# Kernel tuning notes

Hardware: AMD Instinct MI355X
Metric: run time of the kernel (lower is better)

## Reference

```python
import jax, jax.numpy as jnp
import numpy as np

KV_POOL = 2


def setup_inputs() -> dict:
    key = jax.random.key(0)
    ks = jax.random.split(key, 12)
    B, C1, C2, H, W, D = 8, 256, 512, 64, 64, 64
    s = 0.02
    return {
        "x1": jax.random.normal(ks[0], (B, C1, H, W), jnp.float32),
        "x2": jax.random.normal(ks[1], (B, C2, H, W), jnp.float32),
        "Wq": jax.random.normal(ks[2], (D, C1), jnp.float32) * s,
        "bq": jnp.zeros((D,), jnp.float32),
        "Wk": jax.random.normal(ks[3], (D, C2), jnp.float32) * s,
        "bk": jnp.zeros((D,), jnp.float32),
        "Wv": jax.random.normal(ks[4], (D, C2), jnp.float32) * s,
        "bv": jnp.zeros((D,), jnp.float32),
        "Wo": jax.random.normal(ks[5], (C1, D), jnp.float32) * s,
        "bo": jnp.zeros((C1,), jnp.float32),
    }


def reference(x1, x2, Wq, bq, Wk, bk, Wv, bv, Wo, bo):
    B, C1, H, W = x1.shape
    D = Wq.shape[0]
    # adaptive_avg_pool2d to (H//2, W//2) with even dims == 2x2 mean pool
    Bs, C2, H2, W2 = x2.shape
    x2p = x2.reshape(Bs, C2, H2 // KV_POOL, KV_POOL, W2 // KV_POOL, KV_POOL).mean(axis=(3, 5))
    # 1x1 convs as channel matmuls; flatten spatial dims
    Q = jnp.einsum('bchw,dc->bhwd', x1, Wq).reshape(B, H * W, D) + bq          # [B,N,D]
    K = jnp.einsum('bchw,dc->bhwd', x2p, Wk).reshape(B, -1, D) + bk            # [B,M,D]
    V = jnp.einsum('bchw,dc->bhwd', x2p, Wv).reshape(B, -1, D) + bv            # [B,M,D]
    attn = jax.nn.softmax(jnp.einsum('bnd,bmd->bnm', Q, K), axis=-1)           # [B,N,M]
    out = jnp.einsum('bnm,bmd->bnd', attn, V)                                  # [B,N,D]
    y = jnp.einsum('bnd,cd->bnc', out, Wo) + bo                                # [B,N,C1]
    y = y.reshape(B, H, W, C1).transpose(0, 3, 1, 2)                           # [B,C1,H,W]
    return x1 + y
```

## Files before the change

kernel.cpp:

```cpp
#include <hip/hip_runtime.h>
#include <hip/hip_bf16.h>

typedef __bf16 bf16x4 __attribute__((ext_vector_type(4)));
typedef __bf16 bf16x8 __attribute__((ext_vector_type(8)));
typedef float f32x16 __attribute__((ext_vector_type(16)));
typedef unsigned int u32x4 __attribute__((ext_vector_type(4)));

static constexpr int Bc = 8, C1 = 256, C2 = 512, Hh = 64, Ww = 64, Dd = 64;
static constexpr int Nn = 4096, Mm = 1024;

#define MFMA __builtin_amdgcn_mfma_f32_32x32x16_bf16

__device__ __forceinline__ uint32_t pkbf(float a, float b) {
  union { __bf16 h[2]; uint32_t u; } x;
  x.h[0] = (__bf16)a; x.h[1] = (__bf16)b;
  return x.u;
}

__device__ __forceinline__ bf16x8 cvt8(const float* __restrict__ p) {
  float4 a = *(const float4*)p;
  float4 b2 = *(const float4*)(p + 4);
  bf16x8 r;
  r[0] = (__bf16)a.x; r[1] = (__bf16)a.y; r[2] = (__bf16)a.z; r[3] = (__bf16)a.w;
  r[4] = (__bf16)b2.x; r[5] = (__bf16)b2.y; r[6] = (__bf16)b2.z; r[7] = (__bf16)b2.w;
  return r;
}

__device__ __forceinline__ void pack16(const float* p, bf16x8& f0, bf16x8& f1) {
  uint32_t w01 = pkbf(p[0], p[1]),   w23 = pkbf(p[2], p[3]);
  uint32_t w45 = pkbf(p[4], p[5]),   w67 = pkbf(p[6], p[7]);
  uint32_t w89 = pkbf(p[8], p[9]),   wab = pkbf(p[10], p[11]);
  uint32_t wcd = pkbf(p[12], p[13]), wef = pkbf(p[14], p[15]);
  auto s0 = __builtin_amdgcn_permlane32_swap(w01, w45, false, false);
  auto s1 = __builtin_amdgcn_permlane32_swap(w23, w67, false, false);
  auto s2 = __builtin_amdgcn_permlane32_swap(w89, wcd, false, false);
  auto s3 = __builtin_amdgcn_permlane32_swap(wab, wef, false, false);
  u32x4 q0 = {s0[0], s1[0], s0[1], s1[1]};
  u32x4 q1 = {s2[0], s3[0], s2[1], s3[1]};
  f0 = __builtin_bit_cast(bf16x8, q0);
  f1 = __builtin_bit_cast(bf16x8, q1);
}

__global__ __launch_bounds__(256) void k_prep_w(
    const float* __restrict__ Wq, const float* __restrict__ Wk,
    const float* __restrict__ Wv, const float* __restrict__ Wo,
    __bf16* __restrict__ wqf, __bf16* __restrict__ wkf,
    __bf16* __restrict__ wvf, __bf16* __restrict__ wof) {
  int t = blockIdx.x * 256 + threadIdx.x;
  if (t < 2048) {
    int l = t & 63, g = t >> 6;
    int dh = g >> 4, ks = g & 15;
    int d = dh * 32 + (l & 31), c = ks * 16 + (l >> 5) * 8;
    *(bf16x8*)(wqf + (size_t)t * 8) = cvt8(Wq + (size_t)d * C1 + c);
  } else if (t < 6144) {
    int tt = t - 2048;
    int l = tt & 63, g = tt >> 6;
    int dh = g >> 5, ks = g & 31;
    int d = dh * 32 + (l & 31), c = ks * 16 + (l >> 5) * 8;
    *(bf16x8*)(wkf + (size_t)tt * 8) = cvt8(Wk + (size_t)d * C2 + c);
  } else if (t < 10240) {
    int tt = t - 6144;
    int l = tt & 63, g = tt >> 6;
    int dh = g >> 5, ks = g & 31;
    int d = dh * 32 + (l & 31), c = ks * 16 + (l >> 5) * 8;
    *(bf16x8*)(wvf + (size_t)tt * 8) = cvt8(Wv + (size_t)d * C2 + c);
  } else if (t < 12288) {
    int tt = t - 10240;
    int l = tt & 63, g = tt >> 6;
    int ct = g >> 2, ks = g & 3;
    int crow = ct * 32 + (l & 31), d = ks * 16 + (l >> 5) * 8;
    *(bf16x8*)(wof + (size_t)tt * 8) = cvt8(Wo + (size_t)crow * Dd + d);
  }
}

__global__ __launch_bounds__(256) void k_proj(
    const float* __restrict__ x1, const float* __restrict__ x2,
    const __bf16* __restrict__ wqf, const float* __restrict__ bq,
    const __bf16* __restrict__ wkf, const float* __restrict__ bk,
    const __bf16* __restrict__ wvf, const float* __restrict__ bv,
    __bf16* __restrict__ qfb, __bf16* __restrict__ kfb,
    __bf16* __restrict__ vfb) {
  __shared__ __align__(16) __bf16 lds[19392];
  const int bx = blockIdx.x, b = blockIdx.y, tid = threadIdx.x;
  const int w = tid >> 6, l = tid & 63, h = l >> 5, nl = l & 31;

  if (bx < 64) {
    const int n0 = bx * 64;
#pragma unroll 4
    for (int it = 0; it < 16; ++it) {
      int c = it * 16 + (tid >> 4);
      int q = tid & 15;
      float4 v = *(const float4*)(x1 + (size_t)(b * C1 + c) * Nn + n0 + 4 * q);
      lds[(4 * q + 0) * 266 + c] = (__bf16)v.x;
      lds[(4 * q + 1) * 266 + c] = (__bf16)v.y;
      lds[(4 * q + 2) * 266 + c] = (__bf16)v.z;
      lds[(4 * q + 3) * 266 + c] = (__bf16)v.w;
    }
    __syncthreads();
    const int nsub = w & 1, dh = w >> 1;
    const __bf16* arow = lds + (nsub * 32 + nl) * 266;
    const __bf16* wq8 = wqf + (size_t)dh * 16 * 512 + l * 8;
    f32x16 acc = {};
#pragma unroll
    for (int ks = 0; ks < 16; ++ks) {
      bf16x8 a = *(const bf16x8*)(arow + ks * 16 + 8 * h);
      bf16x8 bb = *(const bf16x8*)(wq8 + ks * 512);
      acc = MFMA(a, bb, acc, 0, 0, 0);
    }
    const int d = dh * 32 + nl;
    const float bias = bq[d];
    __bf16* qdst = qfb + (size_t)b * Nn * Dd + (size_t)((n0 >> 5) + nsub) * 2048 +
                   (d >> 4) * 512 + ((d >> 3) & 1) * 256 + (d & 7);
#pragma unroll
    for (int r = 0; r < 16; ++r) {
      int mrow = (r & 3) + 8 * (r >> 2) + 4 * h;
      qdst[mrow * 8] = (__bf16)(acc[r] + bias);
    }
  } else {
    const int h2 = bx - 64;
    __bf16* klds = lds;
    __bf16* vlds = lds + 32 * 522;
#pragma unroll 4
    for (int it = 0; it < 64; ++it) {
      int c = it * 8 + (tid >> 5);
      int j = tid & 31;
      const float* p = x2 + ((size_t)(b * C2 + c) * Hh + 2 * h2) * Ww + 2 * j;
      float2 v0 = *(const float2*)p;
      float2 v1 = *(const float2*)(p + Ww);
      klds[j * 522 + c] = (__bf16)((v0.x + v0.y + v1.x + v1.y) * 0.25f);
    }
    __syncthreads();
    const int isv = w >> 1, dh = w & 1;
    const __bf16* arow = klds + nl * 522;
    const __bf16* wf8 = (isv ? wvf : wkf) + (size_t)dh * 32 * 512 + l * 8;
    f32x16 acc = {};
#pragma unroll
    for (int ks = 0; ks < 32; ++ks) {
      bf16x8 a = *(const bf16x8*)(arow + ks * 16 + 8 * h);
      bf16x8 bb = *(const bf16x8*)(wf8 + ks * 512);
      acc = MFMA(a, bb, acc, 0, 0, 0);
    }
    const int d = dh * 32 + nl;
    const float bias = isv ? bv[d] : bk[d];
    if (!isv) {
      __bf16* kdst = kfb + (size_t)b * Mm * Dd + (size_t)h2 * 2048 +
                     (d >> 4) * 512 + ((d >> 3) & 1) * 256 + (d & 7);
#pragma unroll
      for (int r = 0; r < 16; ++r) {
        int mr = (r & 3) + 8 * (r >> 2) + 4 * h;
        kdst[mr * 8] = (__bf16)(acc[r] + bias);
      }
    } else {
#pragma unroll
      for (int r = 0; r < 16; ++r) {
        int mr = (r & 3) + 8 * (r >> 2) + 4 * h;
        vlds[d * 42 + mr] = (__bf16)(acc[r] + bias);
      }
    }
    __syncthreads();
    const int dd = tid >> 2, q = tid & 3;
    bf16x8 vv = *(const bf16x8*)(vlds + dd * 42 + q * 8);
    const int c = (q >> 1) * 2 + (dd >> 5);
    const int ll = (q & 1) * 32 + (dd & 31);
    *(bf16x8*)(vfb + (size_t)b * Mm * Dd + (size_t)h2 * 2048 + c * 512 + ll * 8) = vv;
  }
}

template <int S>
__global__ __launch_bounds__(256) void k_attn_part(
    const __bf16* __restrict__ qfb, const __bf16* __restrict__ kfb,
    const __bf16* __restrict__ vfb, __bf16* __restrict__ po,
    float* __restrict__ pml) {
  const int lin = blockIdx.x;
  const int b = lin & 7, rest = lin >> 3, nblk = rest & 31, sp = rest >> 5;
  const int tid = threadIdx.x;
  const int w = tid >> 6, l = tid & 63, h = l >> 5, nl = l & 31;
  const int n = nblk * 128 + w * 32 + nl;
  constexpr int NT = Mm / S / 32;
  const int t0 = sp * NT;

  const __bf16* qt = qfb + (size_t)b * Nn * Dd + (size_t)(nblk * 4 + w) * 2048 + l * 8;
  bf16x8 qf0 = *(const bf16x8*)(qt);
  bf16x8 qf1 = *(const bf16x8*)(qt + 512);
  bf16x8 qf2 = *(const bf16x8*)(qt + 1024);
  bf16x8 qf3 = *(const bf16x8*)(qt + 1536);

  const __bf16* kt = kfb + (size_t)b * Mm * Dd + (size_t)t0 * 2048 + l * 8;
  const __bf16* vt = vfb + (size_t)b * Mm * Dd + (size_t)t0 * 2048 + l * 8;

  f32x16 o0 = {}, o1 = {};
  float lsum = 0.f;

  bf16x8 ck0 = *(const bf16x8*)(kt);
  bf16x8 ck1 = *(const bf16x8*)(kt + 512);
  bf16x8 ck2 = *(const bf16x8*)(kt + 1024);
  bf16x8 ck3 = *(const bf16x8*)(kt + 1536);
  bf16x8 cv0 = *(const bf16x8*)(vt);
  bf16x8 cv1 = *(const bf16x8*)(vt + 512);
  bf16x8 cv2 = *(const bf16x8*)(vt + 1024);
  bf16x8 cv3 = *(const bf16x8*)(vt + 1536);

#pragma unroll
  for (int i = 0; i < NT; ++i) {
    bf16x8 nk0, nk1, nk2, nk3, nv0, nv1, nv2, nv3;
    if (i + 1 < NT) {
      const __bf16* kn = kt + (size_t)(i + 1) * 2048;
      const __bf16* vn = vt + (size_t)(i + 1) * 2048;
      nk0 = *(const bf16x8*)(kn);
      nk1 = *(const bf16x8*)(kn + 512);
      nk2 = *(const bf16x8*)(kn + 1024);
      nk3 = *(const bf16x8*)(kn + 1536);
      nv0 = *(const bf16x8*)(vn);
      nv1 = *(const bf16x8*)(vn + 512);
      nv2 = *(const bf16x8*)(vn + 1024);
      nv3 = *(const bf16x8*)(vn + 1536);
    }
    f32x16 s = {};
    s = MFMA(ck0, qf0, s, 0, 0, 0);
    s = MFMA(ck1, qf1, s, 0, 0, 0);
    s = MFMA(ck2, qf2, s, 0, 0, 0);
    s = MFMA(ck3, qf3, s, 0, 0, 0);
    float p[16];
#pragma unroll
    for (int r = 0; r < 16; ++r) p[r] = __expf(s[r]);
    float u0 = (p[0] + p[1]) + (p[2] + p[3]);
    float u1 = (p[4] + p[5]) + (p[6] + p[7]);
    float u2 = (p[8] + p[9]) + (p[10] + p[11]);
    float u3 = (p[12] + p[13]) + (p[14] + p[15]);
    lsum += (u0 + u1) + (u2 + u3);
    bf16x8 pb0, pb1;
    pack16(p, pb0, pb1);
    o0 = MFMA(cv0, pb0, o0, 0, 0, 0);
    o1 = MFMA(cv1, pb0, o1, 0, 0, 0);
    o0 = MFMA(cv2, pb1, o0, 0, 0, 0);
    o1 = MFMA(cv3, pb1, o1, 0, 0, 0);
    if (i + 1 < NT) {
      ck0 = nk0; ck1 = nk1; ck2 = nk2; ck3 = nk3;
      cv0 = nv0; cv1 = nv1; cv2 = nv2; cv3 = nv3;
    }
  }

  const float ltot = lsum + __shfl_xor(lsum, 32);
  __bf16* ob = po + (size_t)(b * S + sp) * 16 * Nn * 4 + (size_t)n * 4;
#pragma unroll
  for (int q = 0; q < 4; ++q) {
    bf16x4 t0v, t1v;
#pragma unroll
    for (int e = 0; e < 4; ++e) {
      t0v[e] = (__bf16)o0[q * 4 + e];
      t1v[e] = (__bf16)o1[q * 4 + e];
    }
    *(bf16x4*)(ob + (size_t)(2 * q + h) * Nn * 4) = t0v;
    *(bf16x4*)(ob + (size_t)(8 + 2 * q + h) * Nn * 4) = t1v;
  }
  if (h == 0) pml[(size_t)(b * S + sp) * Nn + n] = ltot;
}

template <int S>
__global__ __launch_bounds__(256) void k_attn_comb(
    const float* __restrict__ x1, const __bf16* __restrict__ po,
    const float* __restrict__ pml, const __bf16* __restrict__ wof,
    const float* __restrict__ bo, float* __restrict__ out) {
  const int lin = blockIdx.x;
  const int b = lin & 7, rest = lin >> 3, nblk = rest & 31, ctg = rest >> 5;
  const int tid = threadIdx.x;
  const int w = tid >> 6, l = tid & 63, h = l >> 5, nl = l & 31;
  const int n = nblk * 128 + w * 32 + nl;

  float L = 0.f;
#pragma unroll
  for (int s = 0; s < S; ++s)
    L += pml[(size_t)(b * S + s) * Nn + n];
  const float inv = 1.f / L;

  float o[32];
#pragma unroll
  for (int r = 0; r < 32; ++r) o[r] = 0.f;
#pragma unroll
  for (int s = 0; s < S; ++s) {
    const __bf16* ob = po + (size_t)(b * S + s) * 16 * Nn * 4 + (size_t)n * 4;
#pragma unroll
    for (int q = 0; q < 4; ++q) {
      bf16x4 v0 = *(const bf16x4*)(ob + (size_t)(2 * q + h) * Nn * 4);
      bf16x4 v1 = *(const bf16x4*)(ob + (size_t)(8 + 2 * q + h) * Nn * 4);
#pragma unroll
      for (int e = 0; e < 4; ++e) {
        o[q * 4 + e] += (float)v0[e];
        o[16 + q * 4 + e] += (float)v1[e];
      }
    }
  }

  bf16x8 obf[4];
#pragma unroll
  for (int a2 = 0; a2 < 2; ++a2) {
    float ov[16];
#pragma unroll
    for (int r = 0; r < 16; ++r) ov[r] = o[a2 * 16 + r] * inv;
    pack16(ov, obf[a2 * 2], obf[a2 * 2 + 1]);
  }

  const float* x1r = x1 + (size_t)b * C1 * Nn + n;
  float* outr = out + (size_t)b * C1 * Nn + n;
#pragma unroll
  for (int ci = 0; ci < 4; ++ci) {
    const int ct = ctg * 4 + ci;
    f32x16 y = {};
#pragma unroll
    for (int ks = 0; ks < 4; ++ks) {
      bf16x8 a = *(const bf16x8*)(wof + (size_t)((ct * 4 + ks) * 64 + l) * 8);
      y = MFMA(a, obf[ks], y, 0, 0, 0);
    }
#pragma unroll
    for (int r = 0; r < 16; ++r) {
      int c = ct * 32 + (r & 3) + 8 * (r >> 2) + 4 * h;
      size_t idx = (size_t)c * Nn;
      outr[idx] = y[r] + bo[c] + x1r[idx];
    }
  }
}

__global__ __launch_bounds__(256) void k_attn(
    const float* __restrict__ x1, const __bf16* __restrict__ qfb,
    const __bf16* __restrict__ kfb, const __bf16* __restrict__ vfb,
    const __bf16* __restrict__ wof, const float* __restrict__ bo,
    float* __restrict__ out) {
  const int b = blockIdx.y, tid = threadIdx.x;
  const int w = tid >> 6, l = tid & 63, h = l >> 5, nl = l & 31;
  const int n = blockIdx.x * 128 + w * 32 + nl;

  const __bf16* qt = qfb + (size_t)b * Nn * Dd + (size_t)(blockIdx.x * 4 + w) * 2048 + l * 8;
  bf16x8 qf0 = *(const bf16x8*)(qt);
  bf16x8 qf1 = *(const bf16x8*)(qt + 512);
  bf16x8 qf2 = *(const bf16x8*)(qt + 1024);
  bf16x8 qf3 = *(const bf16x8*)(qt + 1536);

  f32x16 o0 = {}, o1 = {};
  float mrun = -INFINITY, lsum = 0.f;

  const __bf16* kb_ = kfb + (size_t)b * Mm * Dd + l * 8;
  const __bf16* vb_ = vfb + (size_t)b * Mm * Dd + l * 8;

  for (int t = 0; t < 32; ++t) {
    const __bf16* kt = kb_ + (size_t)t * 2048;
    const __bf16* vt = vb_ + (size_t)t * 2048;
    bf16x8 ka0 = *(const bf16x8*)(kt);
    bf16x8 ka1 = *(const bf16x8*)(kt + 512);
    bf16x8 ka2 = *(const bf16x8*)(kt + 1024);
    bf16x8 ka3 = *(const bf16x8*)(kt + 1536);
    bf16x8 v00 = *(const bf16x8*)(vt);
    bf16x8 v10 = *(const bf16x8*)(vt + 512);
    bf16x8 v01 = *(const bf16x8*)(vt + 1024);
    bf16x8 v11 = *(const bf16x8*)(vt + 1536);
    f32x16 s = {};
    s = MFMA(ka0, qf0, s, 0, 0, 0);
    s = MFMA(ka1, qf1, s, 0, 0, 0);
    s = MFMA(ka2, qf2, s, 0, 0, 0);
    s = MFMA(ka3, qf3, s, 0, 0, 0);
    float tmax = s[0];
#pragma unroll
    for (int r = 1; r < 16; ++r) tmax = fmaxf(tmax, s[r]);
    tmax = fmaxf(tmax, __shfl_xor(tmax, 32));
    const float mnew = fmaxf(mrun, tmax);
    const float scale = __expf(mrun - mnew);
    float p[16], psum = 0.f;
#pragma unroll
    for (int r = 0; r < 16; ++r) { p[r] = __expf(s[r] - mnew); psum += p[r]; }
    lsum = lsum * scale + psum;
    mrun = mnew;
#pragma unroll
    for (int r = 0; r < 16; ++r) { o0[r] *= scale; o1[r] *= scale; }
    bf16x8 pb0, pb1;
    pack16(p, pb0, pb1);
    o0 = MFMA(v00, pb0, o0, 0, 0, 0);
    o1 = MFMA(v10, pb0, o1, 0, 0, 0);
    o0 = MFMA(v01, pb1, o0, 0, 0, 0);
    o1 = MFMA(v11, pb1, o1, 0, 0, 0);
  }

  const float ltot = lsum + __shfl_xor(lsum, 32);
  const float inv = 1.f / ltot;

  bf16x8 ob[4];
#pragma unroll
  for (int a2 = 0; a2 < 2; ++a2) {
    float ov[16];
#pragma unroll
    for (int r = 0; r < 16; ++r) ov[r] = (a2 ? o1[r] : o0[r]) * inv;
    pack16(ov, ob[a2 * 2], ob[a2 * 2 + 1]);
  }

  const float* x1r = x1 + (size_t)b * C1 * Nn + n;
  float* outr = out + (size_t)b * C1 * Nn + n;
#pragma unroll 2
  for (int ct = 0; ct < 8; ++ct) {
    f32x16 y = {};
#pragma unroll
    for (int ks = 0; ks < 4; ++ks) {
      bf16x8 a = *(const bf16x8*)(wof + (size_t)((ct * 4 + ks) * 64 + l) * 8);
      y = MFMA(a, ob[ks], y, 0, 0, 0);
    }
#pragma unroll
    for (int r = 0; r < 16; ++r) {
      int c = ct * 32 + (r & 3) + 8 * (r >> 2) + 4 * h;
      size_t idx = (size_t)c * Nn;
      outr[idx] = y[r] + bo[c] + x1r[idx];
    }
  }
}

extern "C" void kernel_launch(void* const* d_in, const int* in_sizes, int n_in,
                              void* d_out, int out_size, void* d_ws,
                              size_t ws_size, hipStream_t stream) {
  const float* x1 = (const float*)d_in[0];
  const float* x2 = (const float*)d_in[1];
  const float* Wq = (const float*)d_in[2];
  const float* bq = (const float*)d_in[3];
  const float* Wk = (const float*)d_in[4];
  const float* bk = (const float*)d_in[5];
  const float* Wv = (const float*)d_in[6];
  const float* bv = (const float*)d_in[7];
  const float* Wo = (const float*)d_in[8];
  const float* bo = (const float*)d_in[9];
  float* out = (float*)d_out;
  char* ws = (char*)d_ws;

  __bf16* wqf = (__bf16*)(ws);
  __bf16* wkf = (__bf16*)(ws + 32768);
  __bf16* wvf = (__bf16*)(ws + 98304);
  __bf16* wof = (__bf16*)(ws + 163840);
  __bf16* qfb = (__bf16*)(ws + 196608);
  __bf16* kfb = (__bf16*)(ws + 4390912);
  __bf16* vfb = (__bf16*)(ws + 5439488);
  __bf16* po  = (__bf16*)(ws + 6488064);
  const size_t ws8 = 6488064ull + 33554432ull + 1048576ull;
  const size_t ws4 = 6488064ull + 16777216ull + 524288ull;

  hipLaunchKernelGGL(k_prep_w, dim3(48), dim3(256), 0, stream,
                     Wq, Wk, Wv, Wo, wqf, wkf, wvf, wof);
  hipLaunchKernelGGL(k_proj, dim3(96, 8), dim3(256), 0, stream,
                     x1, x2, wqf, bq, wkf, bk, wvf, bv, qfb, kfb, vfb);
  if (ws_size >= ws8) {
    float* pml = (float*)(ws + 6488064 + 33554432);
    hipLaunchKernelGGL(k_attn_part<8>, dim3(32 * 8 * 8), dim3(256), 0, stream,
                       qfb, kfb, vfb, po, pml);
    hipLaunchKernelGGL(k_attn_comb<8>, dim3(32 * 8 * 2), dim3(256), 0, stream,
                       x1, po, pml, wof, bo, out);
  } else if (ws_size >= ws4) {
    float* pml = (float*)(ws + 6488064 + 16777216);
    hipLaunchKernelGGL(k_attn_part<4>, dim3(32 * 8 * 4), dim3(256), 0, stream,
                       qfb, kfb, vfb, po, pml);
    hipLaunchKernelGGL(k_attn_comb<4>, dim3(32 * 8 * 2), dim3(256), 0, stream,
                       x1, po, pml, wof, bo, out);
  } else {
    hipLaunchKernelGGL(k_attn, dim3(32, 8), dim3(256), 0, stream,
                       x1, qfb, kfb, vfb, wof, bo, out);
  }
}
```

Measured before the change: 63.36 us.

## Stage x1 and pooled x2 as bf16 MFMA fragments in a separate wide kernel

Adds a staging kernel that converts x1 and the 2x2-pooled x2 into bf16 fragment-ordered buffers across many small blocks, with weight prep folded into the same launch. The projection kernel then reads MFMA operands straight from global memory with no LDS transpose or syncthreads. The V output is packed with permlane swaps instead of going through LDS. The aim is more parallelism and less LDS traffic in the projection stage. The cost is an extra round trip of about 25MB of bf16 data through global memory and a larger workspace requirement, which may push execution onto the smaller-split fallback paths.

```diff
diff --git a/kernel.cpp b/kernel.cpp
--- a/kernel.cpp
+++ b/kernel.cpp
@@ -41,75 +41,124 @@
   f1 = __builtin_bit_cast(bf16x8, q1);
 }
 
-__global__ __launch_bounds__(256) void k_prep_w(
+
+__global__ __launch_bounds__(256) void k_stage(
+    const float* __restrict__ x1, const float* __restrict__ x2,
     const float* __restrict__ Wq, const float* __restrict__ Wk,
     const float* __restrict__ Wv, const float* __restrict__ Wo,
     __bf16* __restrict__ wqf, __bf16* __restrict__ wkf,
-    __bf16* __restrict__ wvf, __bf16* __restrict__ wof) {
-  int t = blockIdx.x * 256 + threadIdx.x;
-  if (t < 2048) {
-    int l = t & 63, g = t >> 6;
-    int dh = g >> 4, ks = g & 15;
-    int d = dh * 32 + (l & 31), c = ks * 16 + (l >> 5) * 8;
-    *(bf16x8*)(wqf + (size_t)t * 8) = cvt8(Wq + (size_t)d * C1 + c);
-  } else if (t < 6144) {
-    int tt = t - 2048;
-    int l = tt & 63, g = tt >> 6;
-    int dh = g >> 5, ks = g & 31;
-    int d = dh * 32 + (l & 31), c = ks * 16 + (l >> 5) * 8;
-    *(bf16x8*)(wkf + (size_t)tt * 8) = cvt8(Wk + (size_t)d * C2 + c);
-  } else if (t < 10240) {
-    int tt = t - 6144;
-    int l = tt & 63, g = tt >> 6;
-    int dh = g >> 5, ks = g & 31;
-    int d = dh * 32 + (l & 31), c = ks * 16 + (l >> 5) * 8;
-    *(bf16x8*)(wvf + (size_t)tt * 8) = cvt8(Wv + (size_t)d * C2 + c);
-  } else if (t < 12288) {
-    int tt = t - 10240;
-    int l = tt & 63, g = tt >> 6;
-    int ct = g >> 2, ks = g & 3;
-    int crow = ct * 32 + (l & 31), d = ks * 16 + (l >> 5) * 8;
-    *(bf16x8*)(wof + (size_t)tt * 8) = cvt8(Wo + (size_t)crow * Dd + d);
+    __bf16* __restrict__ wvf, __bf16* __restrict__ wof,
+    __bf16* __restrict__ x1f, __bf16* __restrict__ x2pf) {
+  __shared__ __align__(16) __bf16 lds[32 * 132];
+  const int lin = blockIdx.x, tid = threadIdx.x;
+  if (lin >= 4096) {
+    int t = (lin - 4096) * 256 + tid;
+    if (t < 2048) {
+      int l = t & 63, g = t >> 6, dh = g >> 4, ks = g & 15;
+      int d = dh * 32 + (l & 31), c = ks * 16 + (l >> 5) * 8;
+      *(bf16x8*)(wqf + (size_t)t * 8) = cvt8(Wq + (size_t)d * C1 + c);
+    } else if (t < 6144) {
+      int tt = t - 2048;
+      int l = tt & 63, g = tt >> 6, dh = g >> 5, ks = g & 31;
+      int d = dh * 32 + (l & 31), c = ks * 16 + (l >> 5) * 8;
+      *(bf16x8*)(wkf + (size_t)tt * 8) = cvt8(Wk + (size_t)d * C2 + c);
+    } else if (t < 10240) {
+      int tt = t - 6144;
+      int l = tt & 63, g = tt >> 6, dh = g >> 5, ks = g & 31;
+      int d = dh * 32 + (l & 31), c = ks * 16 + (l >> 5) * 8;
+      *(bf16x8*)(wvf + (size_t)tt * 8) = cvt8(Wv + (size_t)d * C2 + c);
+    } else if (t < 12288) {
+      int tt = t - 10240;
+      int l = tt & 63, g = tt >> 6, ct = g >> 2, ks = g & 3;
+      int crow = ct * 32 + (l & 31), d = ks * 16 + (l >> 5) * 8;
+      *(bf16x8*)(wof + (size_t)tt * 8) = cvt8(Wo + (size_t)crow * Dd + d);
+    }
+    return;
+  }
+  const int b = lin & 7, idx = lin >> 3;
+  const int w = tid >> 6, l = tid & 63;
+
+  if (idx < 256) {
+    const int t = idx >> 1, cc = idx & 1;
+    const int n0 = t * 32, c0 = cc * 128;
+#pragma unroll
+    for (int it = 0; it < 4; ++it) {
+      int cl = it * 32 + (tid >> 3);
+      int q = tid & 7;
+      float4 v = *(const float4*)(x1 + (size_t)(b * C1 + c0 + cl) * Nn + n0 + 4 * q);
+      lds[(4 * q + 0) * 132 + cl] = (__bf16)v.x;
+      lds[(4 * q + 1) * 132 + cl] = (__bf16)v.y;
+      lds[(4 * q + 2) * 132 + cl] = (__bf16)v.z;
+      lds[(4 * q + 3) * 132 + cl] = (__bf16)v.w;
+    }
+    __syncthreads();
+#pragma unroll
+    for (int j = 0; j < 2; ++j) {
+      int ks8 = w * 2 + j;
+      int off = (l & 31) * 132 + ks8 * 16 + (l >> 5) * 8;
+      bf16x4 lo = *(const bf16x4*)(lds + off);
+      bf16x4 hi = *(const bf16x4*)(lds + off + 4);
+      __bf16* dst = x1f + ((size_t)(b * 128 + t) * 16 + cc * 8 + ks8) * 512 + l * 8;
+      *(bf16x4*)dst = lo;
+      *(bf16x4*)(dst + 4) = hi;
+    }
+  } else {
+    const int idx2 = idx - 256;
+    const int t = idx2 >> 3, cc = idx2 & 7;
+    const int c0 = cc * 64;
+    const int g = tid >> 4, lane16 = tid & 15, row = g & 1;
+#pragma unroll
+    for (int it = 0; it < 8; ++it) {
+      int cl = it * 8 + (g >> 1);
+      const float* p =
+          x2 + ((size_t)(b * C2 + c0 + cl) * Hh + 2 * t + row) * Ww + 4 * lane16;
+      float4 v = *(const float4*)p;
+      float s0 = v.x + v.y, s1 = v.z + v.w;
+      float p0 = (s0 + __shfl_xor(s0, 16)) * 0.25f;
+      float p1 = (s1 + __shfl_xor(s1, 16)) * 0.25f;
+      if (row == 0) {
+        lds[(2 * lane16) * 68 + cl] = (__bf16)p0;
+        lds[(2 * lane16 + 1) * 68 + cl] = (__bf16)p1;
+      }
+    }
+    __syncthreads();
+    const int ks8 = w;
+    int off = (l & 31) * 68 + ks8 * 16 + (l >> 5) * 8;
+    bf16x4 lo = *(const bf16x4*)(lds + off);
+    bf16x4 hi = *(const bf16x4*)(lds + off + 4);
+    __bf16* dst = x2pf + ((size_t)(b * 32 + t) * 32 + cc * 4 + ks8) * 512 + l * 8;
+    *(bf16x4*)dst = lo;
+    *(bf16x4*)(dst + 4) = hi;
   }
 }
 
 __global__ __launch_bounds__(256) void k_proj(
-    const float* __restrict__ x1, const float* __restrict__ x2,
+    const __bf16* __restrict__ x1f, const __bf16* __restrict__ x2pf,
     const __bf16* __restrict__ wqf, const float* __restrict__ bq,
     const __bf16* __restrict__ wkf, const float* __restrict__ bk,
     const __bf16* __restrict__ wvf, const float* __restrict__ bv,
     __bf16* __restrict__ qfb, __bf16* __restrict__ kfb,
     __bf16* __restrict__ vfb) {
-  __shared__ __align__(16) __bf16 lds[19392];
-  const int bx = blockIdx.x, b = blockIdx.y, tid = threadIdx.x;
+  const int lin = blockIdx.x;
+  const int b = lin & 7, idx = lin >> 3;
+  const int tid = threadIdx.x;
   const int w = tid >> 6, l = tid & 63, h = l >> 5, nl = l & 31;
 
-  if (bx < 64) {
-    const int n0 = bx * 64;
-#pragma unroll 4
-    for (int it = 0; it < 16; ++it) {
-      int c = it * 16 + (tid >> 4);
-      int q = tid & 15;
-      float4 v = *(const float4*)(x1 + (size_t)(b * C1 + c) * Nn + n0 + 4 * q);
-      lds[(4 * q + 0) * 266 + c] = (__bf16)v.x;
-      lds[(4 * q + 1) * 266 + c] = (__bf16)v.y;
-      lds[(4 * q + 2) * 266 + c] = (__bf16)v.z;
-      lds[(4 * q + 3) * 266 + c] = (__bf16)v.w;
-    }
-    __syncthreads();
+  if (idx < 64) {
     const int nsub = w & 1, dh = w >> 1;
-    const __bf16* arow = lds + (nsub * 32 + nl) * 266;
-    const __bf16* wq8 = wqf + (size_t)dh * 16 * 512 + l * 8;
+    const int t = idx * 2 + nsub;
+    const __bf16* af = x1f + ((size_t)(b * 128 + t) * 16) * 512 + l * 8;
+    const __bf16* wf = wqf + (size_t)dh * 16 * 512 + l * 8;
     f32x16 acc = {};
 #pragma unroll
     for (int ks = 0; ks < 16; ++ks) {
-      bf16x8 a = *(const bf16x8*)(arow + ks * 16 + 8 * h);
-      bf16x8 bb = *(const bf16x8*)(wq8 + ks * 512);
+      bf16x8 a = *(const bf16x8*)(af + ks * 512);
+      bf16x8 bb = *(const bf16x8*)(wf + ks * 512);
       acc = MFMA(a, bb, acc, 0, 0, 0);
     }
     const int d = dh * 32 + nl;
     const float bias = bq[d];
-    __bf16* qdst = qfb + (size_t)b * Nn * Dd + (size_t)((n0 >> 5) + nsub) * 2048 +
+    __bf16* qdst = qfb + (size_t)b * Nn * Dd + (size_t)t * 2048 +
                    (d >> 4) * 512 + ((d >> 3) & 1) * 256 + (d & 7);
 #pragma unroll
     for (int r = 0; r < 16; ++r) {
@@ -117,32 +166,20 @@
       qdst[mrow * 8] = (__bf16)(acc[r] + bias);
     }
   } else {
-    const int h2 = bx - 64;
-    __bf16* klds = lds;
-    __bf16* vlds = lds + 32 * 522;
-#pragma unroll 4
-    for (int it = 0; it < 64; ++it) {
-      int c = it * 8 + (tid >> 5);
-      int j = tid & 31;
-      const float* p = x2 + ((size_t)(b * C2 + c) * Hh + 2 * h2) * Ww + 2 * j;
-      float2 v0 = *(const float2*)p;
-      float2 v1 = *(const float2*)(p + Ww);
-      klds[j * 522 + c] = (__bf16)((v0.x + v0.y + v1.x + v1.y) * 0.25f);
-    }
-    __syncthreads();
+    const int h2 = idx - 64;
     const int isv = w >> 1, dh = w & 1;
-    const __bf16* arow = klds + nl * 522;
-    const __bf16* wf8 = (isv ? wvf : wkf) + (size_t)dh * 32 * 512 + l * 8;
+    const __bf16* af = x2pf + ((size_t)(b * 32 + h2) * 32) * 512 + l * 8;
+    const __bf16* wf = (isv ? wvf : wkf) + (size_t)dh * 32 * 512 + l * 8;
     f32x16 acc = {};
 #pragma unroll
     for (int ks = 0; ks < 32; ++ks) {
-      bf16x8 a = *(const bf16x8*)(arow + ks * 16 + 8 * h);
-      bf16x8 bb = *(const bf16x8*)(wf8 + ks * 512);
+      bf16x8 a = *(const bf16x8*)(af + ks * 512);
+      bf16x8 bb = *(const bf16x8*)(wf + ks * 512);
       acc = MFMA(a, bb, acc, 0, 0, 0);
     }
     const int d = dh * 32 + nl;
-    const float bias = isv ? bv[d] : bk[d];
     if (!isv) {
+      const float bias = bk[d];
       __bf16* kdst = kfb + (size_t)b * Mm * Dd + (size_t)h2 * 2048 +
                      (d >> 4) * 512 + ((d >> 3) & 1) * 256 + (d & 7);
 #pragma unroll
@@ -151,18 +188,16 @@
         kdst[mr * 8] = (__bf16)(acc[r] + bias);
       }
     } else {
-#pragma unroll
-      for (int r = 0; r < 16; ++r) {
-        int mr = (r & 3) + 8 * (r >> 2) + 4 * h;
-        vlds[d * 42 + mr] = (__bf16)(acc[r] + bias);
-      }
-    }
-    __syncthreads();
-    const int dd = tid >> 2, q = tid & 3;
-    bf16x8 vv = *(const bf16x8*)(vlds + dd * 42 + q * 8);
-    const int c = (q >> 1) * 2 + (dd >> 5);
-    const int ll = (q & 1) * 32 + (dd & 31);
-    *(bf16x8*)(vfb + (size_t)b * Mm * Dd + (size_t)h2 * 2048 + c * 512 + ll * 8) = vv;
+      const float bias = bv[d];
+      float ov[16];
+#pragma unroll
+      for (int r = 0; r < 16; ++r) ov[r] = acc[r] + bias;
+      bf16x8 f0, f1;
+      pack16(ov, f0, f1);
+      __bf16* vdst = vfb + (size_t)b * Mm * Dd + (size_t)h2 * 2048 + l * 8;
+      *(bf16x8*)(vdst + (size_t)dh * 512) = f0;
+      *(bf16x8*)(vdst + (size_t)(2 + dh) * 512) = f1;
+    }
   }
 }
 
@@ -425,29 +460,31 @@
   float* out = (float*)d_out;
   char* ws = (char*)d_ws;
 
-  __bf16* wqf = (__bf16*)(ws);
-  __bf16* wkf = (__bf16*)(ws + 32768);
-  __bf16* wvf = (__bf16*)(ws + 98304);
-  __bf16* wof = (__bf16*)(ws + 163840);
-  __bf16* qfb = (__bf16*)(ws + 196608);
-  __bf16* kfb = (__bf16*)(ws + 4390912);
-  __bf16* vfb = (__bf16*)(ws + 5439488);
-  __bf16* po  = (__bf16*)(ws + 6488064);
-  const size_t ws8 = 6488064ull + 33554432ull + 1048576ull;
-  const size_t ws4 = 6488064ull + 16777216ull + 524288ull;
-
-  hipLaunchKernelGGL(k_prep_w, dim3(48), dim3(256), 0, stream,
-                     Wq, Wk, Wv, Wo, wqf, wkf, wvf, wof);
-  hipLaunchKernelGGL(k_proj, dim3(96, 8), dim3(256), 0, stream,
-                     x1, x2, wqf, bq, wkf, bk, wvf, bv, qfb, kfb, vfb);
+  __bf16* wqf  = (__bf16*)(ws);
+  __bf16* wkf  = (__bf16*)(ws + 32768);
+  __bf16* wvf  = (__bf16*)(ws + 98304);
+  __bf16* wof  = (__bf16*)(ws + 163840);
+  __bf16* qfb  = (__bf16*)(ws + 196608);
+  __bf16* kfb  = (__bf16*)(ws + 4390912);
+  __bf16* vfb  = (__bf16*)(ws + 5439488);
+  __bf16* x1f  = (__bf16*)(ws + 6488064);
+  __bf16* x2pf = (__bf16*)(ws + 23265280);
+  __bf16* po   = (__bf16*)(ws + 31653888);
+  const size_t ws8 = 31653888ull + 33554432ull + 1048576ull;
+  const size_t ws4 = 31653888ull + 16777216ull + 524288ull;
+
+  hipLaunchKernelGGL(k_stage, dim3(4144), dim3(256), 0, stream,
+                     x1, x2, Wq, Wk, Wv, Wo, wqf, wkf, wvf, wof, x1f, x2pf);
+  hipLaunchKernelGGL(k_proj, dim3(768), dim3(256), 0, stream,
+                     x1f, x2pf, wqf, bq, wkf, bk, wvf, bv, qfb, kfb, vfb);
   if (ws_size >= ws8) {
-    float* pml = (float*)(ws + 6488064 + 33554432);
+    float* pml = (float*)(ws + 31653888 + 33554432);
     hipLaunchKernelGGL(k_attn_part<8>, dim3(32 * 8 * 8), dim3(256), 0, stream,
                        qfb, kfb, vfb, po, pml);
     hipLaunchKernelGGL(k_attn_comb<8>, dim3(32 * 8 * 2), dim3(256), 0, stream,
                        x1, po, pml, wof, bo, out);
   } else if (ws_size >= ws4) {
-    float* pml = (float*)(ws + 6488064 + 16777216);
+    float* pml = (float*)(ws + 31653888 + 16777216);
     hipLaunchKernelGGL(k_attn_part<4>, dim3(32 * 8 * 4), dim3(256), 0, stream,
                        qfb, kfb, vfb, po, pml);
     hipLaunchKernelGGL(k_attn_comb<4>, dim3(32 * 8 * 2), dim3(256), 0, stream,
```

New measurement: 66.45 us. +4.9%, slower.
